# Kernel optimization log

Hardware: AMD Instinct MI355X
Metric: run time of the kernel (lower is better)

Reference implementation:

```python
import jax, jax.numpy as jnp
import numpy as np

N_NODES = 50000
N_EDGES = 800000
N_GRAPHS = 64


def setup_inputs() -> dict:
    key = jax.random.key(0)
    ks = jax.random.split(key, 13)
    x = jax.random.normal(ks[0], (N_NODES, 1), dtype=jnp.float32)
    edge_index = jax.random.randint(ks[1], (2, N_EDGES), 0, N_NODES)
    batch = jnp.sort(jax.random.randint(ks[2], (N_NODES,), 0, N_GRAPHS))
    def glorot(k, shape):
        fan_in, fan_out = shape
        s = jnp.sqrt(6.0 / (fan_in + fan_out))
        return jax.random.uniform(k, shape, jnp.float32, -s, s)
    W1 = glorot(ks[3], (1, 128));    b1 = jnp.zeros((128,), jnp.float32)
    W2 = glorot(ks[4], (128, 128));  b2 = jnp.zeros((128,), jnp.float32)
    W3 = glorot(ks[5], (128, 256));  b3 = jnp.zeros((256,), jnp.float32)
    Wf1 = glorot(ks[6], (256, 128)); bf1 = jnp.zeros((128,), jnp.float32)
    Wf2 = glorot(ks[7], (128, 10));  bf2 = jnp.zeros((10,), jnp.float32)
    return {"x": x, "edge_index": edge_index, "batch": batch,
            "W1": W1, "b1": b1, "W2": W2, "b2": b2, "W3": W3, "b3": b3,
            "Wf1": Wf1, "bf1": bf1, "Wf2": Wf2, "bf2": bf2}


def _gcn_conv(x, W, b, src, dst, n_nodes):
    # PyG GCNConv: h = X W; out = D^{-1/2} (A + I) D^{-1/2} h + b
    h = x @ W                                  # [N, F_out]
    loop = jnp.arange(n_nodes)
    s = jnp.concatenate([src, loop])           # sources incl. self-loops
    d = jnp.concatenate([dst, loop])           # targets incl. self-loops
    deg = jax.ops.segment_sum(jnp.ones_like(d, h.dtype), d, num_segments=n_nodes)
    dis = jax.lax.rsqrt(jnp.maximum(deg, 1e-12))  # deg >= 1 due to self-loops
    norm = dis[s] * dis[d]                     # [E+N]
    out = jax.ops.segment_sum(h[s] * norm[:, None], d, num_segments=n_nodes)
    return out + b


def reference(x, edge_index, batch, W1, b1, W2, b2, W3, b3, Wf1, bf1, Wf2, bf2):
    src, dst = edge_index[0], edge_index[1]
    n = x.shape[0]
    h = jax.nn.relu(_gcn_conv(x, W1, b1, src, dst, n))
    h = jax.nn.relu(_gcn_conv(h, W2, b2, src, dst, n))
    h = jax.nn.relu(_gcn_conv(h, W3, b3, src, dst, n))   # [N, 256]
    g = jax.ops.segment_max(h, batch, num_segments=N_GRAPHS)  # global_max_pool [G, 256]
    g = jax.nn.relu(g @ Wf1 + bf1)
    # F.dropout with training=self.training: identity in eval mode
    g = g @ Wf2 + bf2
    return jax.nn.relu(g)                       # [G, 10]
```

## Files before the change

kernel.cpp:

```cpp
#include <hip/hip_runtime.h>
#include <hip/hip_bf16.h>

#define N_GRAPHS 64

typedef float f32x4 __attribute__((ext_vector_type(4)));
typedef short bf16x8 __attribute__((ext_vector_type(8)));

__device__ inline unsigned short f2bf(float f) {
    unsigned int u = __float_as_uint(f);
    u = u + 0x7fffu + ((u >> 16) & 1u);
    return (unsigned short)(u >> 16);
}
__device__ inline float bf2f(unsigned short h) {
    return __uint_as_float(((unsigned int)h) << 16);
}

__global__ void k_degpos(const int* __restrict__ dst, int E,
                         int* __restrict__ deg, unsigned short* __restrict__ pos) {
    int e = blockIdx.x * blockDim.x + threadIdx.x;
    if (e < E) pos[e] = (unsigned short)atomicAdd(&deg[dst[e]], 1);
}

__global__ void k_place(const int* __restrict__ src, const int* __restrict__ dst,
                        const unsigned short* __restrict__ pos,
                        const int* __restrict__ row_ptr,
                        int E, unsigned short* __restrict__ csr) {
    int e = blockIdx.x * blockDim.x + threadIdx.x;
    if (e < E) csr[row_ptr[dst[e]] + (int)pos[e]] = (unsigned short)src[e];
}

__global__ void k_dis_bsum(const int* __restrict__ deg, const float* __restrict__ x,
                           float* __restrict__ dis, float* __restrict__ xp,
                           int* __restrict__ bsum, int N) {
    int i = blockIdx.x * 256 + threadIdx.x;
    int dv = (i < N) ? deg[i] : 0;
    if (i < N) {
        float d = rsqrtf((float)(dv + 1));
        dis[i] = d;
        xp[i]  = d * x[i];
    }
    int v = dv;
#pragma unroll
    for (int o = 1; o < 64; o <<= 1) v += __shfl_xor(v, o);
    __shared__ int ws4[4];
    if ((threadIdx.x & 63) == 0) ws4[threadIdx.x >> 6] = v;
    __syncthreads();
    if (threadIdx.x == 0) bsum[blockIdx.x] = ws4[0] + ws4[1] + ws4[2] + ws4[3];
}

__device__ inline int block_scan_inc(int v, int* wsum) {
    int lane = threadIdx.x & 63, w = threadIdx.x >> 6;
    int iv = v;
#pragma unroll
    for (int o = 1; o < 64; o <<= 1) {
        int t = __shfl_up(iv, o);
        if (lane >= o) iv += t;
    }
    if (lane == 63) wsum[w] = iv;
    __syncthreads();
    int add = 0;
    for (int k = 0; k < w; ++k) add += wsum[k];
    return iv + add;
}

__global__ void k_scan_sums(const int* __restrict__ bsum, int nb, int* __restrict__ boff) {
    __shared__ int wsum[4];
    int tid = threadIdx.x;
    int v = (tid < nb) ? bsum[tid] : 0;
    int inc = block_scan_inc(v, wsum);
    if (tid < nb) boff[tid] = inc - v;
}

__global__ void k_scan_apply(const int* __restrict__ deg, const int* __restrict__ boff,
                             int* __restrict__ row_ptr, int N) {
    __shared__ int wsum[4];
    int b = blockIdx.x, i = b * 256 + threadIdx.x;
    int v = (i < N) ? deg[i] : 0;
    int inc = block_scan_inc(v, wsum) + boff[b];
    if (i < N) {
        row_ptr[i] = inc - v;
        if (i == N - 1) row_ptr[N] = inc;
    }
}

__global__ void k_agg_scalar(const float* __restrict__ xp, const float* __restrict__ dis,
                             const int* __restrict__ row_ptr,
                             const unsigned short* __restrict__ csr,
                             float2* __restrict__ td2, int N) {
    int d = blockIdx.x * blockDim.x + threadIdx.x;
    if (d >= N) return;
    float acc = xp[d];
    int e0 = row_ptr[d], e1 = row_ptr[d + 1];
    int e = e0;
    for (; e + 8 <= e1; e += 8) {
        int s0 = csr[e],     s1 = csr[e + 1], s2 = csr[e + 2], s3 = csr[e + 3];
        int s4 = csr[e + 4], s5 = csr[e + 5], s6 = csr[e + 6], s7 = csr[e + 7];
        acc += ((xp[s0] + xp[s1]) + (xp[s2] + xp[s3]))
             + ((xp[s4] + xp[s5]) + (xp[s6] + xp[s7]));
    }
    for (; e < e1; ++e) acc += xp[csr[e]];
    float dd = dis[d];
    td2[d] = make_float2(dd * acc, dd);
}

__global__ void k_h1agg(const float2* __restrict__ td2,
                        const float4* __restrict__ W1f4, const float4* __restrict__ b1f4,
                        const int* __restrict__ row_ptr,
                        const unsigned short* __restrict__ csr,
                        float4* __restrict__ out4, int N) {
    int node = blockIdx.x * 8 + (threadIdx.x >> 5);
    int lane = threadIdx.x & 31;
    if (node >= N) return;
    const float4 w1 = W1f4[lane];
    const float4 bv = b1f4[lane];
    float2 sv = td2[node];
    float dd = sv.y;
    float a0 = dd * fmaxf(fmaf(sv.x, w1.x, bv.x), 0.f);
    float a1 = dd * fmaxf(fmaf(sv.x, w1.y, bv.y), 0.f);
    float a2 = dd * fmaxf(fmaf(sv.x, w1.z, bv.z), 0.f);
    float a3 = dd * fmaxf(fmaf(sv.x, w1.w, bv.w), 0.f);
    int e0 = row_ptr[node], e1 = row_ptr[node + 1];
    int e = e0;
    for (; e + 8 <= e1; e += 8) {
        int s0 = csr[e],     s1 = csr[e + 1], s2 = csr[e + 2], s3 = csr[e + 3];
        int s4 = csr[e + 4], s5 = csr[e + 5], s6 = csr[e + 6], s7 = csr[e + 7];
        float2 v0 = td2[s0], v1 = td2[s1], v2 = td2[s2], v3 = td2[s3];
        float2 v4 = td2[s4], v5 = td2[s5], v6 = td2[s6], v7 = td2[s7];
        a0 += ((v0.y * fmaxf(fmaf(v0.x, w1.x, bv.x), 0.f)
              + v1.y * fmaxf(fmaf(v1.x, w1.x, bv.x), 0.f))
             + (v2.y * fmaxf(fmaf(v2.x, w1.x, bv.x), 0.f)
              + v3.y * fmaxf(fmaf(v3.x, w1.x, bv.x), 0.f)))
            + ((v4.y * fmaxf(fmaf(v4.x, w1.x, bv.x), 0.f)
              + v5.y * fmaxf(fmaf(v5.x, w1.x, bv.x), 0.f))
             + (v6.y * fmaxf(fmaf(v6.x, w1.x, bv.x), 0.f)
              + v7.y * fmaxf(fmaf(v7.x, w1.x, bv.x), 0.f)));
        a1 += ((v0.y * fmaxf(fmaf(v0.x, w1.y, bv.y), 0.f)
              + v1.y * fmaxf(fmaf(v1.x, w1.y, bv.y), 0.f))
             + (v2.y * fmaxf(fmaf(v2.x, w1.y, bv.y), 0.f)
              + v3.y * fmaxf(fmaf(v3.x, w1.y, bv.y), 0.f)))
            + ((v4.y * fmaxf(fmaf(v4.x, w1.y, bv.y), 0.f)
              + v5.y * fmaxf(fmaf(v5.x, w1.y, bv.y), 0.f))
             + (v6.y * fmaxf(fmaf(v6.x, w1.y, bv.y), 0.f)
              + v7.y * fmaxf(fmaf(v7.x, w1.y, bv.y), 0.f)));
        a2 += ((v0.y * fmaxf(fmaf(v0.x, w1.z, bv.z), 0.f)
              + v1.y * fmaxf(fmaf(v1.x, w1.z, bv.z), 0.f))
             + (v2.y * fmaxf(fmaf(v2.x, w1.z, bv.z), 0.f)
              + v3.y * fmaxf(fmaf(v3.x, w1.z, bv.z), 0.f)))
            + ((v4.y * fmaxf(fmaf(v4.x, w1.z, bv.z), 0.f)
              + v5.y * fmaxf(fmaf(v5.x, w1.z, bv.z), 0.f))
             + (v6.y * fmaxf(fmaf(v6.x, w1.z, bv.z), 0.f)
              + v7.y * fmaxf(fmaf(v7.x, w1.z, bv.z), 0.f)));
        a3 += ((v0.y * fmaxf(fmaf(v0.x, w1.w, bv.w), 0.f)
              + v1.y * fmaxf(fmaf(v1.x, w1.w, bv.w), 0.f))
             + (v2.y * fmaxf(fmaf(v2.x, w1.w, bv.w), 0.f)
              + v3.y * fmaxf(fmaf(v3.x, w1.w, bv.w), 0.f)))
            + ((v4.y * fmaxf(fmaf(v4.x, w1.w, bv.w), 0.f)
              + v5.y * fmaxf(fmaf(v5.x, w1.w, bv.w), 0.f))
             + (v6.y * fmaxf(fmaf(v6.x, w1.w, bv.w), 0.f)
              + v7.y * fmaxf(fmaf(v7.x, w1.w, bv.w), 0.f)));
    }
    for (; e < e1; ++e) {
        float2 v = td2[csr[e]];
        a0 += v.y * fmaxf(fmaf(v.x, w1.x, bv.x), 0.f);
        a1 += v.y * fmaxf(fmaf(v.x, w1.y, bv.y), 0.f);
        a2 += v.y * fmaxf(fmaf(v.x, w1.z, bv.z), 0.f);
        a3 += v.y * fmaxf(fmaf(v.x, w1.w, bv.w), 0.f);
    }
    out4[(size_t)node * 32 + lane] = make_float4(a0 * dd, a1 * dd, a2 * dd, a3 * dd);
}

__global__ void k_agg128h(const float4* __restrict__ hp4, const float* __restrict__ dis,
                          const int* __restrict__ row_ptr,
                          const unsigned short* __restrict__ csr,
                          float4* __restrict__ out4, int N, int half) {
    int node = blockIdx.x * 16 + (threadIdx.x >> 4);
    int lane = threadIdx.x & 15;
    if (node >= N) return;
    const int co = half * 16 + lane;
    float4 self = hp4[(size_t)node * 32 + co];
    float a0 = self.x, a1 = self.y, a2 = self.z, a3 = self.w;
    int e0 = row_ptr[node], e1 = row_ptr[node + 1];
    int e = e0;
    for (; e + 8 <= e1; e += 8) {
        int s0 = csr[e],     s1 = csr[e + 1], s2 = csr[e + 2], s3 = csr[e + 3];
        int s4 = csr[e + 4], s5 = csr[e + 5], s6 = csr[e + 6], s7 = csr[e + 7];
        float4 v0 = hp4[(size_t)s0 * 32 + co];
        float4 v1 = hp4[(size_t)s1 * 32 + co];
        float4 v2 = hp4[(size_t)s2 * 32 + co];
        float4 v3 = hp4[(size_t)s3 * 32 + co];
        float4 v4 = hp4[(size_t)s4 * 32 + co];
        float4 v5 = hp4[(size_t)s5 * 32 + co];
        float4 v6 = hp4[(size_t)s6 * 32 + co];
        float4 v7 = hp4[(size_t)s7 * 32 + co];
        a0 += ((v0.x + v1.x) + (v2.x + v3.x)) + ((v4.x + v5.x) + (v6.x + v7.x));
        a1 += ((v0.y + v1.y) + (v2.y + v3.y)) + ((v4.y + v5.y) + (v6.y + v7.y));
        a2 += ((v0.z + v1.z) + (v2.z + v3.z)) + ((v4.z + v5.z) + (v6.z + v7.z));
        a3 += ((v0.w + v1.w) + (v2.w + v3.w)) + ((v4.w + v5.w) + (v6.w + v7.w));
    }
    for (; e < e1; ++e) {
        int s = csr[e];
        float4 v = hp4[(size_t)s * 32 + co];
        a0 += v.x; a1 += v.y; a2 += v.z; a3 += v.w;
    }
    float d = dis[node];
    f32x4 r = {a0 * d, a1 * d, a2 * d, a3 * d};
    __builtin_nontemporal_store(r, (f32x4*)&out4[(size_t)node * 32 + co]);
}

__global__ void k_wpack2z(const float* __restrict__ W2, const float* __restrict__ W3,
                          unsigned short* __restrict__ Wp2H, unsigned short* __restrict__ Wp2L,
                          unsigned short* __restrict__ Wp3H, unsigned short* __restrict__ Wp3L,
                          int* __restrict__ deg, unsigned int* __restrict__ g, int N) {
    int idx = blockIdx.x * 256 + threadIdx.x;
    if (idx < N) deg[idx] = 0;
    if (idx < N_GRAPHS * 256) g[idx] = 0;
    const float* W; unsigned short *WpH, *WpL; int F, j;
    if (idx < 128 * 128) { W = W2; WpH = Wp2H; WpL = Wp2L; F = 128; j = idx; }
    else if (idx < 128 * 128 + 128 * 256) {
        W = W3; WpH = Wp3H; WpL = Wp3L; F = 256; j = idx - 128 * 128;
    } else return;
    int k = j / F, col = j - k * F;
    float v = W[j];
    unsigned short h = f2bf(v);
    unsigned short l = f2bf(v - bf2f(h));
    int o = ((k >> 3) * F + col) * 8 + (k & 7);
    WpH[o] = h; WpL[o] = l;
}

template<int FOUT, bool SCALE, bool FUSE_MAX>
__global__ __launch_bounds__(256, 3) void k_gemm_mfma(
        const float* __restrict__ A,
        const unsigned short* __restrict__ WpH, const unsigned short* __restrict__ WpL,
        const float* __restrict__ b, const float* __restrict__ dis,
        float* __restrict__ outp, const int* __restrict__ batch,
        unsigned int* __restrict__ gmax, int N) {
    __shared__ __align__(16) unsigned short ApH[4 * 4 * 16 * 8];
    __shared__ __align__(16) unsigned short ApL[4 * 4 * 16 * 8];
    __shared__ __align__(16) unsigned short WlH[4 * 128 * 8];
    __shared__ __align__(16) unsigned short WlL[4 * 128 * 8];
    const int tid  = threadIdx.x;
    const int lane = tid & 63;
    const int w    = tid >> 6;
    const int n0   = blockIdx.x * 64;
    const int jh   = blockIdx.y;

    f32x4 acc[8];
#pragma unroll
    for (int ct = 0; ct < 8; ++ct) acc[ct] = (f32x4){0.f, 0.f, 0.f, 0.f};

    for (int kc = 0; kc < 128; kc += 32) {
#pragma unroll
        for (int it = 0; it < 2; ++it) {
            int q = tid + it * 256;
            int kg = q >> 7, cq = q & 127;
            int src = ((kc >> 3) + kg) * FOUT + jh * 128 + cq;
            ((f32x4*)WlH)[q] = ((const f32x4*)WpH)[src];
            ((f32x4*)WlL)[q] = ((const f32x4*)WpL)[src];
        }
#pragma unroll
        for (int it = 0; it < 2; ++it) {
            int idx = tid + it * 256;
            int node = idx >> 3, k4 = idx & 7;
            int gn = n0 + node;
            float4 a = (gn < N)
                ? *reinterpret_cast<const float4*>(A + (size_t)gn * 128 + kc + k4 * 4)
                : make_float4(0.f, 0.f, 0.f, 0.f);
            unsigned short h0 = f2bf(a.x), h1 = f2bf(a.y), h2 = f2bf(a.z), h3 = f2bf(a.w);
            unsigned short l0 = f2bf(a.x - bf2f(h0)), l1 = f2bf(a.y - bf2f(h1));
            unsigned short l2 = f2bf(a.z - bf2f(h2)), l3 = f2bf(a.w - bf2f(h3));
            int kg = k4 >> 1, e0 = (k4 & 1) * 4;
            int base = (((node >> 4) * 4 + kg) * 16 + (node & 15)) * 8 + e0;
            *reinterpret_cast<ushort4*>(&ApH[base]) = make_ushort4(h0, h1, h2, h3);
            *reinterpret_cast<ushort4*>(&ApL[base]) = make_ushort4(l0, l1, l2, l3);
        }
        __syncthreads();

        int aidx = (w * 4 + (lane >> 4)) * 16 + (lane & 15);
        bf16x8 aH = ((const bf16x8*)ApH)[aidx];
        bf16x8 aL = ((const bf16x8*)ApL)[aidx];
#pragma unroll
        for (int ct = 0; ct < 8; ++ct) {
            int bidx = (lane >> 4) * 128 + ct * 16 + (lane & 15);
            bf16x8 bH = ((const bf16x8*)WlH)[bidx];
            bf16x8 bL = ((const bf16x8*)WlL)[bidx];
            acc[ct] = __builtin_amdgcn_mfma_f32_16x16x32_bf16(aL, bL, acc[ct], 0, 0, 0);
            acc[ct] = __builtin_amdgcn_mfma_f32_16x16x32_bf16(aL, bH, acc[ct], 0, 0, 0);
            acc[ct] = __builtin_amdgcn_mfma_f32_16x16x32_bf16(aH, bL, acc[ct], 0, 0, 0);
            acc[ct] = __builtin_amdgcn_mfma_f32_16x16x32_bf16(aH, bH, acc[ct], 0, 0, 0);
        }
        __syncthreads();
    }

    const int cl = lane & 15;
    const int r0 = (lane >> 4) * 4;
    float bb[8];
#pragma unroll
    for (int ct = 0; ct < 8; ++ct) bb[ct] = b[jh * 128 + ct * 16 + cl];

    if (!FUSE_MAX) {
#pragma unroll
        for (int r = 0; r < 4; ++r) {
            int node = n0 + w * 16 + r0 + r;
            if (node < N) {
                float dsc = SCALE ? dis[node] : 1.f;
                float* op = outp + (size_t)node * FOUT + jh * 128 + cl;
#pragma unroll
                for (int ct = 0; ct < 8; ++ct) {
                    float v = fmaxf(acc[ct][r] + bb[ct], 0.f);
                    op[ct * 16] = SCALE ? v * dsc : v;
                }
            }
        }
    } else {
        int nbm[4];
#pragma unroll
        for (int r = 0; r < 4; ++r) {
            int node = n0 + w * 16 + r0 + r;
            nbm[r] = (node < N) ? batch[node] : -1;
        }
        int gfirst = batch[n0];
        int glast  = batch[min(n0 + 63, N - 1)];
        for (int gb = gfirst; gb <= glast; ++gb) {
#pragma unroll
            for (int ct = 0; ct < 8; ++ct) {
                float m = 0.f;
#pragma unroll
                for (int r = 0; r < 4; ++r) {
                    float v = fmaxf(acc[ct][r] + bb[ct], 0.f);
                    if (nbm[r] == gb) m = fmaxf(m, v);
                }
                m = fmaxf(m, __shfl_xor(m, 16));
                m = fmaxf(m, __shfl_xor(m, 32));
                if ((lane >> 4) == 0)
                    atomicMax(&gmax[gb * 256 + jh * 128 + ct * 16 + cl],
                              __float_as_uint(m));
            }
        }
    }
}

__global__ void k_mlp(const float* __restrict__ g, const float* __restrict__ Wf1,
                      const float* __restrict__ bf1, const float* __restrict__ Wf2,
                      const float* __restrict__ bf2, float* __restrict__ out) {
    __shared__ float gr[256];
    __shared__ float g1s[128];
    const int gid = blockIdx.x;
    const int tid = threadIdx.x;
    gr[tid] = g[gid * 256 + tid];
    gr[tid + 128] = g[gid * 256 + 128 + tid];
    __syncthreads();
    float acc = bf1[tid];
    for (int k = 0; k < 256; ++k)
        acc = fmaf(gr[k], Wf1[k * 128 + tid], acc);
    g1s[tid] = fmaxf(acc, 0.f);
    __syncthreads();
    if (tid < 10) {
        float a = bf2[tid];
        for (int k = 0; k < 128; ++k)
            a = fmaf(g1s[k], Wf2[k * 10 + tid], a);
        out[gid * 10 + tid] = fmaxf(a, 0.f);
    }
}

extern "C" void kernel_launch(void* const* d_in, const int* in_sizes, int n_in,
                              void* d_out, int out_size, void* d_ws, size_t ws_size,
                              hipStream_t stream) {
    const float* x   = (const float*)d_in[0];
    const int*   ei  = (const int*)d_in[1];
    const int*   bat = (const int*)d_in[2];
    const float* W1  = (const float*)d_in[3];
    const float* b1  = (const float*)d_in[4];
    const float* W2  = (const float*)d_in[5];
    const float* b2  = (const float*)d_in[6];
    const float* W3  = (const float*)d_in[7];
    const float* b3  = (const float*)d_in[8];
    const float* Wf1 = (const float*)d_in[9];
    const float* bf1 = (const float*)d_in[10];
    const float* Wf2 = (const float*)d_in[11];
    const float* bf2 = (const float*)d_in[12];
    float* out = (float*)d_out;

    const int N = in_sizes[0];
    const int E = in_sizes[1] / 2;
    const int* src = ei;
    const int* dst = ei + E;

    char* base = (char*)d_ws;
    size_t off = 0;
    auto carve = [&](size_t bytes) -> char* {
        char* p = base + off;
        off = (off + bytes + 255) & ~(size_t)255;
        return p;
    };
    const int nb = (N + 255) / 256;
    int*    deg     = (int*)   carve((size_t)N * 4);
    unsigned short* epos = (unsigned short*)carve((size_t)E * 2);
    int*    row_ptr = (int*)   carve((size_t)(N + 1) * 4);
    unsigned short* csr = (unsigned short*)carve((size_t)E * 2);
    float*  dis     = (float*) carve((size_t)N * 4);
    float*  xp      = (float*) carve((size_t)N * 4);
    float2* td2     = (float2*)carve((size_t)N * 8);
    float*  A2      = (float*) carve((size_t)N * 128 * 4);
    float*  B2      = (float*) carve((size_t)N * 128 * 4);
    float*  A3      = (float*) carve((size_t)N * 128 * 4);
    unsigned int* g = (unsigned int*)carve((size_t)N_GRAPHS * 256 * 4);
    int*    bsum    = (int*)   carve((size_t)nb * 4);
    int*    boff    = (int*)   carve((size_t)nb * 4);
    unsigned short* Wp2H = (unsigned short*)carve((size_t)128 * 128 * 2);
    unsigned short* Wp2L = (unsigned short*)carve((size_t)128 * 128 * 2);
    unsigned short* Wp3H = (unsigned short*)carve((size_t)128 * 256 * 2);
    unsigned short* Wp3L = (unsigned short*)carve((size_t)128 * 256 * 2);
    (void)ws_size; (void)n_in; (void)out_size;

    int eb = (E + 255) / 256;

    k_wpack2z<<<nb, 256, 0, stream>>>(W2, W3, Wp2H, Wp2L, Wp3H, Wp3L, deg, g, N);

    k_degpos<<<eb, 256, 0, stream>>>(dst, E, deg, epos);
    k_dis_bsum<<<nb, 256, 0, stream>>>(deg, x, dis, xp, bsum, N);
    k_scan_sums<<<1, 256, 0, stream>>>(bsum, nb, boff);
    k_scan_apply<<<nb, 256, 0, stream>>>(deg, boff, row_ptr, N);
    k_place<<<eb, 256, 0, stream>>>(src, dst, epos, row_ptr, E, csr);

    k_agg_scalar<<<nb, 256, 0, stream>>>(xp, dis, row_ptr, csr, td2, N);

    const int gx = (N + 63) / 64;
    const int ab = (N + 7) / 8;
    const int ab16 = (N + 15) / 16;

    k_h1agg<<<ab, 256, 0, stream>>>(td2, (const float4*)W1, (const float4*)b1,
                                    row_ptr, csr, (float4*)A2, N);
    k_gemm_mfma<128, true, false><<<dim3(gx, 1), 256, 0, stream>>>(
        A2, Wp2H, Wp2L, b2, dis, B2, nullptr, nullptr, N);

    k_agg128h<<<ab16, 256, 0, stream>>>((const float4*)B2, dis, row_ptr, csr,
                                        (float4*)A3, N, 0);
    k_agg128h<<<ab16, 256, 0, stream>>>((const float4*)B2, dis, row_ptr, csr,
                                        (float4*)A3, N, 1);
    k_gemm_mfma<256, false, true><<<dim3(gx, 2), 256, 0, stream>>>(
        A3, Wp3H, Wp3L, b3, nullptr, nullptr, bat, g, N);

    k_mlp<<<N_GRAPHS, 128, 0, stream>>>((const float*)g, Wf1, bf1, Wf2, bf2, out);
}
```

Before: 207.3 us.

## Split layer-3 aggregation into quarters, pack dst with position, fold scan kernel

```diff
diff --git a/kernel.cpp b/kernel.cpp
--- a/kernel.cpp
+++ b/kernel.cpp
@@ -16,17 +16,26 @@
 }
 
 __global__ void k_degpos(const int* __restrict__ dst, int E,
-                         int* __restrict__ deg, unsigned short* __restrict__ pos) {
+                         int* __restrict__ deg, unsigned int* __restrict__ combo) {
     int e = blockIdx.x * blockDim.x + threadIdx.x;
-    if (e < E) pos[e] = (unsigned short)atomicAdd(&deg[dst[e]], 1);
-}
-
-__global__ void k_place(const int* __restrict__ src, const int* __restrict__ dst,
-                        const unsigned short* __restrict__ pos,
+    if (e < E) {
+        int d = dst[e];
+        unsigned int p = (unsigned int)atomicAdd(&deg[d], 1);
+        combo[e] = (p << 16) | (unsigned int)d;
+    }
+}
+
+__global__ void k_place(const int* __restrict__ src,
+                        const unsigned int* __restrict__ combo,
                         const int* __restrict__ row_ptr,
                         int E, unsigned short* __restrict__ csr) {
     int e = blockIdx.x * blockDim.x + threadIdx.x;
-    if (e < E) csr[row_ptr[dst[e]] + (int)pos[e]] = (unsigned short)src[e];
+    if (e < E) {
+        unsigned int c = combo[e];
+        int d = (int)(c & 0xffffu);
+        int p = (int)(c >> 16);
+        csr[row_ptr[d] + p] = (unsigned short)src[e];
+    }
 }
 
 __global__ void k_dis_bsum(const int* __restrict__ deg, const float* __restrict__ x,
@@ -63,20 +72,15 @@
     return iv + add;
 }
 
-__global__ void k_scan_sums(const int* __restrict__ bsum, int nb, int* __restrict__ boff) {
-    __shared__ int wsum[4];
-    int tid = threadIdx.x;
-    int v = (tid < nb) ? bsum[tid] : 0;
-    int inc = block_scan_inc(v, wsum);
-    if (tid < nb) boff[tid] = inc - v;
-}
-
-__global__ void k_scan_apply(const int* __restrict__ deg, const int* __restrict__ boff,
+__global__ void k_scan_apply(const int* __restrict__ deg, const int* __restrict__ bsum,
                              int* __restrict__ row_ptr, int N) {
     __shared__ int wsum[4];
     int b = blockIdx.x, i = b * 256 + threadIdx.x;
     int v = (i < N) ? deg[i] : 0;
-    int inc = block_scan_inc(v, wsum) + boff[b];
+    int inc = block_scan_inc(v, wsum);
+    int boff = 0;
+    for (int k = 0; k < b; ++k) boff += bsum[k];
+    inc += boff;
     if (i < N) {
         row_ptr[i] = inc - v;
         if (i == N - 1) row_ptr[N] = inc;
@@ -169,14 +173,14 @@
     out4[(size_t)node * 32 + lane] = make_float4(a0 * dd, a1 * dd, a2 * dd, a3 * dd);
 }
 
-__global__ void k_agg128h(const float4* __restrict__ hp4, const float* __restrict__ dis,
+__global__ void k_agg128q(const float4* __restrict__ hp4, const float* __restrict__ dis,
                           const int* __restrict__ row_ptr,
                           const unsigned short* __restrict__ csr,
-                          float4* __restrict__ out4, int N, int half) {
-    int node = blockIdx.x * 16 + (threadIdx.x >> 4);
-    int lane = threadIdx.x & 15;
+                          float4* __restrict__ out4, int N, int quarter) {
+    int node = blockIdx.x * 32 + (threadIdx.x >> 3);
+    int lane = threadIdx.x & 7;
     if (node >= N) return;
-    const int co = half * 16 + lane;
+    const int co = quarter * 8 + lane;
     float4 self = hp4[(size_t)node * 32 + co];
     float a0 = self.x, a1 = self.y, a2 = self.z, a3 = self.w;
     int e0 = row_ptr[node], e1 = row_ptr[node + 1];
@@ -394,7 +398,7 @@
     };
     const int nb = (N + 255) / 256;
     int*    deg     = (int*)   carve((size_t)N * 4);
-    unsigned short* epos = (unsigned short*)carve((size_t)E * 2);
+    unsigned int* combo = (unsigned int*)carve((size_t)E * 4);
     int*    row_ptr = (int*)   carve((size_t)(N + 1) * 4);
     unsigned short* csr = (unsigned short*)carve((size_t)E * 2);
     float*  dis     = (float*) carve((size_t)N * 4);
@@ -405,7 +409,6 @@
     float*  A3      = (float*) carve((size_t)N * 128 * 4);
     unsigned int* g = (unsigned int*)carve((size_t)N_GRAPHS * 256 * 4);
     int*    bsum    = (int*)   carve((size_t)nb * 4);
-    int*    boff    = (int*)   carve((size_t)nb * 4);
     unsigned short* Wp2H = (unsigned short*)carve((size_t)128 * 128 * 2);
     unsigned short* Wp2L = (unsigned short*)carve((size_t)128 * 128 * 2);
     unsigned short* Wp3H = (unsigned short*)carve((size_t)128 * 256 * 2);
@@ -416,27 +419,25 @@
 
     k_wpack2z<<<nb, 256, 0, stream>>>(W2, W3, Wp2H, Wp2L, Wp3H, Wp3L, deg, g, N);
 
-    k_degpos<<<eb, 256, 0, stream>>>(dst, E, deg, epos);
+    k_degpos<<<eb, 256, 0, stream>>>(dst, E, deg, combo);
     k_dis_bsum<<<nb, 256, 0, stream>>>(deg, x, dis, xp, bsum, N);
-    k_scan_sums<<<1, 256, 0, stream>>>(bsum, nb, boff);
-    k_scan_apply<<<nb, 256, 0, stream>>>(deg, boff, row_ptr, N);
-    k_place<<<eb, 256, 0, stream>>>(src, dst, epos, row_ptr, E, csr);
+    k_scan_apply<<<nb, 256, 0, stream>>>(deg, bsum, row_ptr, N);
+    k_place<<<eb, 256, 0, stream>>>(src, combo, row_ptr, E, csr);
 
     k_agg_scalar<<<nb, 256, 0, stream>>>(xp, dis, row_ptr, csr, td2, N);
 
     const int gx = (N + 63) / 64;
     const int ab = (N + 7) / 8;
-    const int ab16 = (N + 15) / 16;
+    const int ab32 = (N + 31) / 32;
 
     k_h1agg<<<ab, 256, 0, stream>>>(td2, (const float4*)W1, (const float4*)b1,
                                     row_ptr, csr, (float4*)A2, N);
     k_gemm_mfma<128, true, false><<<dim3(gx, 1), 256, 0, stream>>>(
         A2, Wp2H, Wp2L, b2, dis, B2, nullptr, nullptr, N);
 
-    k_agg128h<<<ab16, 256, 0, stream>>>((const float4*)B2, dis, row_ptr, csr,
-                                        (float4*)A3, N, 0);
-    k_agg128h<<<ab16, 256, 0, stream>>>((const float4*)B2, dis, row_ptr, csr,
-                                        (float4*)A3, N, 1);
+    for (int q = 0; q < 4; ++q)
+        k_agg128q<<<ab32, 256, 0, stream>>>((const float4*)B2, dis, row_ptr, csr,
+                                            (float4*)A3, N, q);
     k_gemm_mfma<256, false, true><<<dim3(gx, 2), 256, 0, stream>>>(
         A3, Wp3H, Wp3L, b3, nullptr, nullptr, bat, g, N);
 
```

After: 209.2 us. Within noise of the previous version (+0.9%).
